# Kernel optimization log

Measured on AMD Instinct MI355X. Metric: run time of the kernel, lower is better.

The kernel has to match this reference:

```python
import jax, jax.numpy as jnp
import numpy as np

N = 50000      # total nodes after flattening [1,1,N,D]
E = 600000     # random edges (plus N self-loops appended)
D = 128        # in_dim == out_dim
H = 8          # num_heads
DP = D // H    # per-head dim (each_out_dim)
SLOPE = 0.2    # DGL GATv2Conv default negative_slope


def setup_inputs() -> dict:
    key = jax.random.key(0)
    ks = jax.random.split(key, 6)
    x = jax.random.normal(ks[0], (1, 1, N, D), dtype=jnp.float32)
    s = 1.0 / np.sqrt(D).astype(np.float32)
    # GATv2Conv params: separate src/dst linear projections (share_weights=False),
    # with bias, plus a per-head attention vector.
    w_src = jax.random.uniform(ks[1], (D, H * DP), jnp.float32, -s, s)
    b_src = jnp.zeros((H * DP,), jnp.float32)
    w_dst = jax.random.uniform(ks[2], (D, H * DP), jnp.float32, -s, s)
    b_dst = jnp.zeros((H * DP,), jnp.float32)
    attn_w = jax.random.uniform(ks[3], (H, DP), jnp.float32, -s, s)
    self_loop = jnp.arange(N, dtype=jnp.int32)
    src = jnp.concatenate([jax.random.randint(ks[4], (E,), 0, N, dtype=jnp.int32), self_loop])
    dst = jnp.concatenate([jax.random.randint(ks[5], (E,), 0, N, dtype=jnp.int32), self_loop])
    return {"x": x, "w_src": w_src, "b_src": b_src, "w_dst": w_dst,
            "b_dst": b_dst, "attn_w": attn_w, "src": src, "dst": dst}


def reference(x, w_src, b_src, w_dst, b_dst, attn_w, src, dst):
    shape = x.shape
    h = x.reshape(-1, shape[3])                       # (N, D)
    n = h.shape[0]
    fs = (h @ w_src + b_src).reshape(n, H, DP)        # (N, H, Dp) source proj
    fd = (h @ w_dst + b_dst).reshape(n, H, DP)        # (N, H, Dp) dest proj
    # GATv2: e_ij = a^T LeakyReLU(W_s h_i + W_d h_j)
    e = jax.nn.leaky_relu(fs[src] + fd[dst], SLOPE)   # (E, H, Dp)
    logits = jnp.einsum('ehd,hd->eh', e, attn_w)      # (E, H)
    # segment softmax over incoming edges of each destination node
    m = jax.ops.segment_max(logits, dst, num_segments=n)
    m = jnp.where(jnp.isfinite(m), m, 0.0)
    ex = jnp.exp(logits - m[dst])                     # (E, H)
    denom = jax.ops.segment_sum(ex, dst, num_segments=n)
    alpha = ex / denom[dst]                           # (E, H)
    # weighted scatter-add aggregation of source features
    out = jax.ops.segment_sum(alpha[:, :, None] * fs[src], dst, num_segments=n)
    return out.reshape(shape)
```

## Files before the change

### kernel.cpp

```cpp
#include <hip/hip_runtime.h>
#include <hip/hip_bf16.h>

#define HH 8
#define DP 16
#define DD 128
#define SLOPE 0.2f

typedef __attribute__((ext_vector_type(8))) short bf16x8;
typedef __attribute__((ext_vector_type(4))) float f32x4;

__device__ __forceinline__ unsigned short f2bf(float f) {
  unsigned u = __float_as_uint(f);
  unsigned r = (u + 0x7FFFu + ((u >> 16) & 1u)) >> 16;
  return (unsigned short)r;
}

__global__ __launch_bounds__(256) void wconv_kernel(const float* __restrict__ w_src,
                                                    const float* __restrict__ w_dst,
                                                    unsigned short* __restrict__ wt) {
  int i = blockIdx.x * 256 + threadIdx.x;
  int cg = i >> 7, k = i & 127;
  float v = (cg < DD) ? w_src[k * DD + cg] : w_dst[k * DD + (cg - DD)];
  wt[i] = f2bf(v);
}

#define BN 64
#define LDK 136
__global__ __launch_bounds__(256) void proj_mfma_count_kernel(
    const float* __restrict__ x, const unsigned short* __restrict__ wt,
    const float* __restrict__ b_src, const float* __restrict__ b_dst,
    float* __restrict__ fs, float* __restrict__ fd, int n,
    const int* __restrict__ dst, int* __restrict__ count, int ecount) {
  __shared__ __align__(16) unsigned short xs[BN * LDK];
  const int tid = threadIdx.x;
  const int block0 = blockIdx.x * BN;

  for (int i = tid; i < BN * 32; i += 256) {
    int m = i >> 5;
    int kq = (i & 31) << 2;
    int node = block0 + m;
    float4 v = make_float4(0.f, 0.f, 0.f, 0.f);
    if (node < n) v = *reinterpret_cast<const float4*>(x + (size_t)node * DD + kq);
    ushort4 h;
    h.x = f2bf(v.x); h.y = f2bf(v.y); h.z = f2bf(v.z); h.w = f2bf(v.w);
    *reinterpret_cast<ushort4*>(&xs[m * LDK + kq]) = h;
  }
  __syncthreads();

  const int lane = tid & 63;
  const int wv = tid >> 6;
  const int n0 = wv * 64;
  const int fr = lane & 15;
  const int fq = lane >> 4;

  f32x4 acc[4][4] = {};

#pragma unroll
  for (int kk = 0; kk < DD; kk += 32) {
    bf16x8 a[4], b[4];
#pragma unroll
    for (int mi = 0; mi < 4; ++mi) {
      const unsigned short* p = &xs[(mi * 16 + fr) * LDK + kk + fq * 8];
      a[mi] = *reinterpret_cast<const bf16x8*>(p);
    }
#pragma unroll
    for (int ni = 0; ni < 4; ++ni) {
      const unsigned short* p = &wt[(size_t)(n0 + ni * 16 + fr) * DD + kk + fq * 8];
      b[ni] = *reinterpret_cast<const bf16x8*>(p);
    }
#pragma unroll
    for (int mi = 0; mi < 4; ++mi)
#pragma unroll
      for (int ni = 0; ni < 4; ++ni)
        acc[mi][ni] = __builtin_amdgcn_mfma_f32_16x16x32_bf16(a[mi], b[ni], acc[mi][ni], 0, 0, 0);
  }

#pragma unroll
  for (int ni = 0; ni < 4; ++ni) {
    int cg = n0 + ni * 16 + fr;
    bool issrc = cg < DD;
    int c = issrc ? cg : cg - DD;
    float bias = issrc ? b_src[c] : b_dst[c];
    float* __restrict__ op = issrc ? fs : fd;
#pragma unroll
    for (int mi = 0; mi < 4; ++mi) {
#pragma unroll
      for (int r = 0; r < 4; ++r) {
        int m = block0 + mi * 16 + fq * 4 + r;
        if (m < n) op[(size_t)m * DD + c] = acc[mi][ni][r] + bias;
      }
    }
  }

  const int stride = gridDim.x * 256;
  for (int e = blockIdx.x * 256 + tid; e < ecount; e += stride)
    atomicAdd(&count[dst[e]], 1);
}

__global__ __launch_bounds__(256) void alloc_kernel(const int* __restrict__ count,
                                                    int* __restrict__ cursor,
                                                    int* __restrict__ total, int n) {
  const int lane = threadIdx.x & 63;
  const int wid = threadIdx.x >> 6;
  const int wave = blockIdx.x * 4 + wid;
  const int i0 = wave * 256;

  int excl[4];
  int carry = 0;
#pragma unroll
  for (int j = 0; j < 4; ++j) {
    int i = i0 + j * 64 + lane;
    int v = (i < n) ? count[i] : 0;
    int incl = v;
#pragma unroll
    for (int off = 1; off < 64; off <<= 1) {
      int t = __shfl_up(incl, (unsigned)off, 64);
      if (lane >= off) incl += t;
    }
    excl[j] = carry + incl - v;
    carry += __shfl(incl, 63, 64);
  }
  int base = 0;
  if (lane == 63) base = atomicAdd(total, carry);
  base = __shfl(base, 63, 64);
#pragma unroll
  for (int j = 0; j < 4; ++j) {
    int i = i0 + j * 64 + lane;
    if (i < n) cursor[i] = base + excl[j];
  }
}

__global__ __launch_bounds__(256) void scatter_kernel(const int* __restrict__ src,
                                                      const int* __restrict__ dst,
                                                      int* __restrict__ cursor,
                                                      int* __restrict__ edge_src, int ecount) {
  int e = blockIdx.x * 256 + threadIdx.x;
  if (e < ecount) {
    int pos = atomicAdd(&cursor[dst[e]], 1);
    edge_src[pos] = src[e];
  }
}

__global__ __launch_bounds__(256) void node_kernel(const float* __restrict__ fs,
                                                   const float* __restrict__ fd,
                                                   const float* __restrict__ attn_w,
                                                   const int* __restrict__ cursor,
                                                   const int* __restrict__ count,
                                                   const int* __restrict__ edge_src,
                                                   float* __restrict__ out, int n) {
  const int wid = threadIdx.x >> 6;
  const int lane = threadIdx.x & 63;
  const int node = blockIdx.x * 4 + wid;
  if (node >= n) return;

  const int d0 = lane * 2;
  const float2 aw = *reinterpret_cast<const float2*>(&attn_w[d0]);
  const float2 fdv = *reinterpret_cast<const float2*>(&fd[(size_t)node * DD + d0]);

  const int e1 = __builtin_amdgcn_readfirstlane(cursor[node]);
  const int e0 = e1 - __builtin_amdgcn_readfirstlane(count[node]);

  float mx[4] = {-1e30f, -1e30f, -1e30f, -1e30f};
  float den[4] = {0.f, 0.f, 0.f, 0.f};
  float2 ac[4] = {{0.f, 0.f}, {0.f, 0.f}, {0.f, 0.f}, {0.f, 0.f}};

  auto logit_of = [&](float2 fsv) -> float {
    float t0 = fsv.x + fdv.x; t0 = (t0 > 0.f) ? t0 : t0 * SLOPE;
    float t1 = fsv.y + fdv.y; t1 = (t1 > 0.f) ? t1 : t1 * SLOPE;
    float p = aw.x * t0 + aw.y * t1;
    p += __shfl_xor(p, 1, 64);
    p += __shfl_xor(p, 2, 64);
    p += __shfl_xor(p, 4, 64);
    return p;
  };
  auto upd = [](float& m, float& dn, float2& a, float logit, float2 fsv) {
    float mn = fmaxf(m, logit);
    float sc = __expf(m - mn);
    float p = __expf(logit - mn);
    dn = dn * sc + p;
    a.x = a.x * sc + p * fsv.x;
    a.y = a.y * sc + p * fsv.y;
    m = mn;
  };
  auto gather = [&](int s) -> float2 {
    return *reinterpret_cast<const float2*>(&fs[(size_t)s * DD + d0]);
  };

  int e = e0;
  const int nfull = (e1 - e0) >> 2;
  if (nfull > 0) {
    int i0 = edge_src[e0], i1 = edge_src[e0 + 1];
    int i2 = edge_src[e0 + 2], i3 = edge_src[e0 + 3];
    float2 f0 = gather(i0), f1 = gather(i1), f2 = gather(i2), f3 = gather(i3);
    int b = (1 < nfull) ? e0 + 4 : e0;
    int j0 = edge_src[b], j1 = edge_src[b + 1];
    int j2 = edge_src[b + 2], j3 = edge_src[b + 3];

    for (int g = 1; g < nfull; ++g) {
      float2 h0 = gather(j0), h1 = gather(j1), h2 = gather(j2), h3 = gather(j3);
      int b2 = (g + 1 < nfull) ? e0 + (g + 1) * 4 : e0;
      int k0 = edge_src[b2], k1 = edge_src[b2 + 1];
      int k2 = edge_src[b2 + 2], k3 = edge_src[b2 + 3];
      float l0 = logit_of(f0), l1 = logit_of(f1);
      float l2 = logit_of(f2), l3 = logit_of(f3);
      upd(mx[0], den[0], ac[0], l0, f0);
      upd(mx[1], den[1], ac[1], l1, f1);
      upd(mx[2], den[2], ac[2], l2, f2);
      upd(mx[3], den[3], ac[3], l3, f3);
      f0 = h0; f1 = h1; f2 = h2; f3 = h3;
      j0 = k0; j1 = k1; j2 = k2; j3 = k3;
    }
    float l0 = logit_of(f0), l1 = logit_of(f1);
    float l2 = logit_of(f2), l3 = logit_of(f3);
    upd(mx[0], den[0], ac[0], l0, f0);
    upd(mx[1], den[1], ac[1], l1, f1);
    upd(mx[2], den[2], ac[2], l2, f2);
    upd(mx[3], den[3], ac[3], l3, f3);
    e = e0 + nfull * 4;
  }
  for (; e < e1; ++e) {
    float2 f0 = gather(edge_src[e]);
    float l0 = logit_of(f0);
    upd(mx[0], den[0], ac[0], l0, f0);
  }

  float M = fmaxf(fmaxf(mx[0], mx[1]), fmaxf(mx[2], mx[3]));
  float denom = 0.f, ax = 0.f, ay = 0.f;
#pragma unroll
  for (int j = 0; j < 4; ++j) {
    float s = __expf(mx[j] - M);
    denom += den[j] * s;
    ax += ac[j].x * s;
    ay += ac[j].y * s;
  }

  float inv = (denom > 0.f) ? 1.f / denom : 0.f;
  *reinterpret_cast<float2*>(&out[(size_t)node * DD + d0]) =
      make_float2(ax * inv, ay * inv);
}

extern "C" void kernel_launch(void* const* d_in, const int* in_sizes, int n_in,
                              void* d_out, int out_size, void* d_ws, size_t ws_size,
                              hipStream_t stream) {
  const float* x      = (const float*)d_in[0];
  const float* w_src  = (const float*)d_in[1];
  const float* b_src  = (const float*)d_in[2];
  const float* w_dst  = (const float*)d_in[3];
  const float* b_dst  = (const float*)d_in[4];
  const float* attn_w = (const float*)d_in[5];
  const int* src = (const int*)d_in[6];
  const int* dst = (const int*)d_in[7];
  float* out = (float*)d_out;

  const int n = in_sizes[0] / DD;
  const int ecount = in_sizes[6];

  size_t off = 0;
  float* fs = (float*)((char*)d_ws + off); off += (size_t)n * DD * sizeof(float);
  float* fd = (float*)((char*)d_ws + off); off += (size_t)n * DD * sizeof(float);
  int* edge_src = (int*)((char*)d_ws + off); off += (size_t)ecount * sizeof(int);
  int* cursor   = (int*)((char*)d_ws + off); off += (size_t)n * sizeof(int);
  int* count    = (int*)((char*)d_ws + off); off += (size_t)n * sizeof(int);
  int* total    = (int*)((char*)d_ws + off); off += sizeof(int);
  off = (off + 15) & ~(size_t)15;
  unsigned short* wt = (unsigned short*)((char*)d_ws + off); off += 256 * DD * sizeof(unsigned short);
  (void)ws_size;

  hipMemsetAsync(count, 0, (size_t)(n + 1) * sizeof(int), stream);

  wconv_kernel<<<(256 * DD) / 256, 256, 0, stream>>>(w_src, w_dst, wt);
  const int proj_blocks = (n + BN - 1) / BN;
  proj_mfma_count_kernel<<<proj_blocks, 256, 0, stream>>>(
      x, wt, b_src, b_dst, fs, fd, n, dst, count, ecount);
  alloc_kernel<<<(n + 1023) / 1024, 256, 0, stream>>>(count, cursor, total, n);
  scatter_kernel<<<(ecount + 255) / 256, 256, 0, stream>>>(src, dst, cursor, edge_src, ecount);
  node_kernel<<<(n + 3) / 4, 256, 0, stream>>>(fs, fd, attn_w, cursor, count, edge_src, out, n);
}
```

Measured before the change: 233.5 us.

## Process two edges per wave with float4 lanes and drop online softmax max

The node aggregation kernel now splits each wave into two 32-lane halves. Each half handles a different incoming edge and each lane loads float4 features, with the partial sums combined across halves by a shuffle at the end. The online max rescaling is removed: each edge contributes exp(logit) directly, which saves one exp and the rescale multiplies per edge, but risks overflow if logits get large. The software-prefetched 4-edge pipeline is dropped, and the GEMM epilogue is reorganised to hoist the bias and output-pointer selection out of the store loops.

```diff
diff --git a/kernel.cpp b/kernel.cpp
--- a/kernel.cpp
+++ b/kernel.cpp
@@ -75,19 +75,27 @@
         acc[mi][ni] = __builtin_amdgcn_mfma_f32_16x16x32_bf16(a[mi], b[ni], acc[mi][ni], 0, 0, 0);
   }
 
+  const bool issrc = (n0 < DD);
+  const float* __restrict__ bsrc = issrc ? b_src : b_dst;
+  float* __restrict__ op = issrc ? fs : fd;
+  const int cbase = issrc ? n0 : n0 - DD;
+  float biasv[4];
+  int cc[4];
 #pragma unroll
   for (int ni = 0; ni < 4; ++ni) {
-    int cg = n0 + ni * 16 + fr;
-    bool issrc = cg < DD;
-    int c = issrc ? cg : cg - DD;
-    float bias = issrc ? b_src[c] : b_dst[c];
-    float* __restrict__ op = issrc ? fs : fd;
-#pragma unroll
-    for (int mi = 0; mi < 4; ++mi) {
-#pragma unroll
-      for (int r = 0; r < 4; ++r) {
-        int m = block0 + mi * 16 + fq * 4 + r;
-        if (m < n) op[(size_t)m * DD + c] = acc[mi][ni][r] + bias;
+    cc[ni] = cbase + ni * 16 + fr;
+    biasv[ni] = bsrc[cc[ni]];
+  }
+#pragma unroll
+  for (int mi = 0; mi < 4; ++mi) {
+#pragma unroll
+    for (int r = 0; r < 4; ++r) {
+      int m = block0 + mi * 16 + fq * 4 + r;
+      if (m < n) {
+        size_t base = (size_t)m * DD;
+#pragma unroll
+        for (int ni = 0; ni < 4; ++ni)
+          op[base + cc[ni]] = acc[mi][ni][r] + biasv[ni];
       }
     }
   }
@@ -153,90 +161,62 @@
   const int node = blockIdx.x * 4 + wid;
   if (node >= n) return;
 
-  const int d0 = lane * 2;
-  const float2 aw = *reinterpret_cast<const float2*>(&attn_w[d0]);
-  const float2 fdv = *reinterpret_cast<const float2*>(&fd[(size_t)node * DD + d0]);
+  const int half = lane >> 5;
+  const int hl = lane & 31;
+  const int d0 = hl * 4;
+
+  const float4 aw4 = *reinterpret_cast<const float4*>(&attn_w[d0]);
+  const float4 fdv = *reinterpret_cast<const float4*>(&fd[(size_t)node * DD + d0]);
 
   const int e1 = __builtin_amdgcn_readfirstlane(cursor[node]);
   const int e0 = e1 - __builtin_amdgcn_readfirstlane(count[node]);
-
-  float mx[4] = {-1e30f, -1e30f, -1e30f, -1e30f};
-  float den[4] = {0.f, 0.f, 0.f, 0.f};
-  float2 ac[4] = {{0.f, 0.f}, {0.f, 0.f}, {0.f, 0.f}, {0.f, 0.f}};
-
-  auto logit_of = [&](float2 fsv) -> float {
-    float t0 = fsv.x + fdv.x; t0 = (t0 > 0.f) ? t0 : t0 * SLOPE;
-    float t1 = fsv.y + fdv.y; t1 = (t1 > 0.f) ? t1 : t1 * SLOPE;
-    float p = aw.x * t0 + aw.y * t1;
+  const int deg = e1 - e0;
+  const int npairs = (deg + 1) >> 1;
+  const int nh = npairs >> 1;
+
+  float den0 = 0.f, den1 = 0.f;
+  float4 ac0 = make_float4(0.f, 0.f, 0.f, 0.f);
+  float4 ac1 = make_float4(0.f, 0.f, 0.f, 0.f);
+
+  auto edge_term = [&](int pp, float& den, float4& ac) {
+    int ei = e0 + pp * 2 + half;
+    bool valid = ei < e1;
+    int s = edge_src[valid ? ei : e0];
+    float4 fsv = *reinterpret_cast<const float4*>(&fs[(size_t)s * DD + d0]);
+    float t0 = fsv.x + fdv.x; t0 = t0 > 0.f ? t0 : t0 * SLOPE;
+    float t1 = fsv.y + fdv.y; t1 = t1 > 0.f ? t1 : t1 * SLOPE;
+    float t2 = fsv.z + fdv.z; t2 = t2 > 0.f ? t2 : t2 * SLOPE;
+    float t3 = fsv.w + fdv.w; t3 = t3 > 0.f ? t3 : t3 * SLOPE;
+    float p = aw4.x * t0 + aw4.y * t1 + aw4.z * t2 + aw4.w * t3;
     p += __shfl_xor(p, 1, 64);
     p += __shfl_xor(p, 2, 64);
-    p += __shfl_xor(p, 4, 64);
-    return p;
+    p = valid ? __expf(p) : 0.f;
+    den += p;
+    ac.x += p * fsv.x;
+    ac.y += p * fsv.y;
+    ac.z += p * fsv.z;
+    ac.w += p * fsv.w;
   };
-  auto upd = [](float& m, float& dn, float2& a, float logit, float2 fsv) {
-    float mn = fmaxf(m, logit);
-    float sc = __expf(m - mn);
-    float p = __expf(logit - mn);
-    dn = dn * sc + p;
-    a.x = a.x * sc + p * fsv.x;
-    a.y = a.y * sc + p * fsv.y;
-    m = mn;
-  };
-  auto gather = [&](int s) -> float2 {
-    return *reinterpret_cast<const float2*>(&fs[(size_t)s * DD + d0]);
-  };
-
-  int e = e0;
-  const int nfull = (e1 - e0) >> 2;
-  if (nfull > 0) {
-    int i0 = edge_src[e0], i1 = edge_src[e0 + 1];
-    int i2 = edge_src[e0 + 2], i3 = edge_src[e0 + 3];
-    float2 f0 = gather(i0), f1 = gather(i1), f2 = gather(i2), f3 = gather(i3);
-    int b = (1 < nfull) ? e0 + 4 : e0;
-    int j0 = edge_src[b], j1 = edge_src[b + 1];
-    int j2 = edge_src[b + 2], j3 = edge_src[b + 3];
-
-    for (int g = 1; g < nfull; ++g) {
-      float2 h0 = gather(j0), h1 = gather(j1), h2 = gather(j2), h3 = gather(j3);
-      int b2 = (g + 1 < nfull) ? e0 + (g + 1) * 4 : e0;
-      int k0 = edge_src[b2], k1 = edge_src[b2 + 1];
-      int k2 = edge_src[b2 + 2], k3 = edge_src[b2 + 3];
-      float l0 = logit_of(f0), l1 = logit_of(f1);
-      float l2 = logit_of(f2), l3 = logit_of(f3);
-      upd(mx[0], den[0], ac[0], l0, f0);
-      upd(mx[1], den[1], ac[1], l1, f1);
-      upd(mx[2], den[2], ac[2], l2, f2);
-      upd(mx[3], den[3], ac[3], l3, f3);
-      f0 = h0; f1 = h1; f2 = h2; f3 = h3;
-      j0 = k0; j1 = k1; j2 = k2; j3 = k3;
-    }
-    float l0 = logit_of(f0), l1 = logit_of(f1);
-    float l2 = logit_of(f2), l3 = logit_of(f3);
-    upd(mx[0], den[0], ac[0], l0, f0);
-    upd(mx[1], den[1], ac[1], l1, f1);
-    upd(mx[2], den[2], ac[2], l2, f2);
-    upd(mx[3], den[3], ac[3], l3, f3);
-    e = e0 + nfull * 4;
-  }
-  for (; e < e1; ++e) {
-    float2 f0 = gather(edge_src[e]);
-    float l0 = logit_of(f0);
-    upd(mx[0], den[0], ac[0], l0, f0);
-  }
-
-  float M = fmaxf(fmaxf(mx[0], mx[1]), fmaxf(mx[2], mx[3]));
-  float denom = 0.f, ax = 0.f, ay = 0.f;
-#pragma unroll
-  for (int j = 0; j < 4; ++j) {
-    float s = __expf(mx[j] - M);
-    denom += den[j] * s;
-    ax += ac[j].x * s;
-    ay += ac[j].y * s;
-  }
-
-  float inv = (denom > 0.f) ? 1.f / denom : 0.f;
-  *reinterpret_cast<float2*>(&out[(size_t)node * DD + d0]) =
-      make_float2(ax * inv, ay * inv);
+
+  for (int pp = 0; pp < nh; ++pp) {
+    edge_term(pp, den0, ac0);
+    edge_term(nh + pp, den1, ac1);
+  }
+  if (npairs & 1) edge_term(npairs - 1, den0, ac0);
+
+  float den = den0 + den1;
+  float4 ac = make_float4(ac0.x + ac1.x, ac0.y + ac1.y, ac0.z + ac1.z, ac0.w + ac1.w);
+  den += __shfl_xor(den, 32, 64);
+  ac.x += __shfl_xor(ac.x, 32, 64);
+  ac.y += __shfl_xor(ac.y, 32, 64);
+  ac.z += __shfl_xor(ac.z, 32, 64);
+  ac.w += __shfl_xor(ac.w, 32, 64);
+
+  if (half == 0) {
+    float inv = (den > 0.f) ? 1.f / den : 0.f;
+    *reinterpret_cast<float4*>(&out[(size_t)node * DD + d0]) =
+        make_float4(ac.x * inv, ac.y * inv, ac.z * inv, ac.w * inv);
+  }
 }
 
 extern "C" void kernel_launch(void* const* d_in, const int* in_sizes, int n_in,
```

After: 222.7 us. -4.6%, faster.
